# Kernel optimization log

Measured on AMD Instinct MI355X. Metric: run time of the kernel, lower is better.

Reference implementation:

```python
import jax, jax.numpy as jnp
import numpy as np

N, M, NBR = 20000, 12, 64
AF, ORIG, H, B, K = 256, 92, 256, 200, 50
N_CONV = 3
EPS = 1e-5


def _bn_train(x, gamma, beta):
    mu = x.mean(0)
    var = x.var(0)  # biased, matches torch BN normalization in train mode
    return (x - mu) * jax.lax.rsqrt(var + EPS) * gamma + beta


def _conv_layer(atom_in, nbr_fea, nbr_idx, w1, b1, w2, b2, gamma, beta):
    n, m = nbr_idx.shape
    m1 = m // 2
    atom_nbr = atom_in[nbr_idx]                     # [N, M, AF]
    atom_u = jnp.broadcast_to(atom_in[:, None, :], (n, m1, atom_in.shape[-1]))
    an1, an2 = atom_nbr[:, :m1], atom_nbr[:, m1:]
    nf1, nf2 = nbr_fea[:, :m1], nbr_fea[:, m1:]
    u1 = jnp.concatenate([atom_u, an1, nf1], axis=2)  # [N, M1, 2*AF+NBR]
    u2 = jnp.concatenate([atom_u, an2, nf2], axis=2)
    g1 = jax.nn.relu(jnp.einsum('nmf,fo->nmo', u1, w1) + b1)
    g2 = jax.nn.softplus(jnp.einsum('nmf,fo->nmo', u2, w1) + b1)
    nbr_sumed = g1.sum(1) + g2.sum(1)               # sum over all M neighbors, [N, 2*AF]
    nbr_sumed = nbr_sumed @ w2 + b2                 # [N, AF]
    nbr_sumed = _bn_train(nbr_sumed, gamma, beta)
    return jax.nn.softplus(atom_in + nbr_sumed)


def setup_inputs() -> dict:
    key = jax.random.key(0)
    ks = jax.random.split(key, 16)
    inp = {
        'atom_fea': jax.random.normal(ks[0], (N, ORIG), jnp.float32),
        'nbr_fea': jax.random.normal(ks[1], (N, M, NBR), jnp.float32),
        'nbr_fea_idx': jax.random.randint(ks[2], (N, M), 0, N),
        'M1_index': jax.random.randint(ks[3], (B * K,), 0, N),
        'seg_ids': jnp.repeat(jnp.arange(B), K),
        'm2_fea': jax.random.normal(ks[4], (B, 4), jnp.float32),
        'emb_w': jax.random.normal(ks[5], (ORIG, AF), jnp.float32) * 0.05,
        'emb_b': jnp.zeros((AF,), jnp.float32),
        'w1': jax.random.normal(ks[6], (N_CONV, 2 * AF + NBR, 2 * AF), jnp.float32) * 0.05,
        'b1': jnp.zeros((N_CONV, 2 * AF), jnp.float32),
        'w2': jax.random.normal(ks[7], (N_CONV, 2 * AF, AF), jnp.float32) * 0.05,
        'b2': jnp.zeros((N_CONV, AF), jnp.float32),
        'gamma': jnp.ones((N_CONV, AF), jnp.float32),
        'beta': jnp.zeros((N_CONV, AF), jnp.float32),
        'fc_w': jax.random.normal(ks[8], (AF + 4, H), jnp.float32) * 0.05,
        'fc_b': jnp.zeros((H,), jnp.float32),
        'out_w': jax.random.normal(ks[9], (H, 1), jnp.float32) * 0.05,
        'out_b': jnp.zeros((1,), jnp.float32),
    }
    return inp


def reference(atom_fea, nbr_fea, nbr_fea_idx, M1_index, seg_ids, m2_fea,
              emb_w, emb_b, w1, b1, w2, b2, gamma, beta,
              fc_w, fc_b, out_w, out_b):
    x = jax.nn.softplus(atom_fea @ emb_w + emb_b)           # [N, AF]
    for i in range(N_CONV):
        x = _conv_layer(x, nbr_fea, nbr_fea_idx, w1[i], b1[i], w2[i], b2[i], gamma[i], beta[i])
    m1_fea = x[M1_index]                                    # [B*K, AF]
    sums = jax.ops.segment_sum(m1_fea, seg_ids, num_segments=B)
    counts = jax.ops.segment_sum(jnp.ones((m1_fea.shape[0], 1), m1_fea.dtype), seg_ids, num_segments=B)
    crys = sums / counts                                    # per-crystal mean, [B, AF]
    crys = jnp.concatenate([crys, m2_fea], axis=1)          # [B, AF+4]
    h = jax.nn.softplus(jax.nn.softplus(crys) @ fc_w + fc_b)
    out = h @ out_w + out_b                                 # [B, 1]
    return out
```

## Files before the change

kernel.cpp:

```cpp
#include <hip/hip_runtime.h>
#include <hip/hip_bf16.h>


#define N_ATOM 20000
#define AF     256
#define F2     512
#define ORIG   92
#define ORIG_P 96
#define BB     200
#define KK     50
#define BN_EPS 1e-5f
#define ZS     132

#define OFF_B1   0
#define OFF_B2   1536
#define OFF_GAM  2304
#define OFF_BET  3072
#define OFF_EMBB 3840
#define OFF_FCB  4096
#define OFF_FCW  4352
#define OFF_OW   70912
#define OFF_OB   71168
#define OFF_M2   71169
#define N_SMALL  71969

#define S_AF   (N_ATOM * ORIG_P)
#define S_EMB  (AF * ORIG_P)
#define S_W12  (3 * 1024 * 256)
#define S_W1F  (3 * 512 * 64)
#define S_W2   (3 * AF * F2)
#define S_SM   N_SMALL
#define S_TOT  (S_AF + S_EMB + S_W12 + S_W1F + S_W2 + S_SM)

using bf16x8 = __attribute__((ext_vector_type(8))) short;
using f32x4  = __attribute__((ext_vector_type(4))) float;

__device__ __forceinline__ float bf2f(__hip_bfloat16 v) { return __bfloat162float(v); }
__device__ __forceinline__ __hip_bfloat16 f2bf(float v) { return __float2bfloat16(v); }
__device__ __forceinline__ unsigned short f2bfbits(float f) {
    unsigned u = __float_as_uint(f);
    u += 0x7fffu + ((u >> 16) & 1u);
    return (unsigned short)(u >> 16);
}
__device__ __forceinline__ float bfbits2f(unsigned short u) {
    return __uint_as_float(((unsigned)u) << 16);
}
__device__ __forceinline__ float softplus_f(float x) {
    return fmaxf(x, 0.f) + __logf(1.f + __expf(-fabsf(x)));
}
__device__ __forceinline__ float ld_any(const void* p, long idx, bool isf32) {
    return isf32 ? ((const float*)p)[idx] : bf2f(((const __hip_bfloat16*)p)[idx]);
}

__global__ void detect_dtype(const unsigned* __restrict__ gamma_raw,
                             unsigned* __restrict__ flag) {
    unsigned u = gamma_raw[0];
    flag[0] = ((u & 0xFFFFu) == 0u) ? 1u : 0u;
}

__global__ __launch_bounds__(256)
void prep_all(const void* af, const void* emb_w, const void* w1, const void* w2,
              const void* b1, const void* b2, const void* gam, const void* bet,
              const void* embb, const void* fcb, const void* fcw,
              const void* ow, const void* ob, const void* m2,
              const unsigned* __restrict__ dflag,
              __hip_bfloat16* __restrict__ af_pad, __hip_bfloat16* __restrict__ embT,
              __hip_bfloat16* __restrict__ w1T2, __hip_bfloat16* __restrict__ w1Tf,
              __hip_bfloat16* __restrict__ w2T, __hip_bfloat16* __restrict__ smalls) {
    bool isf32 = dflag[0] != 0u;
    int i = blockIdx.x * 256 + threadIdx.x;
    if (i < S_AF) {
        int r = i / ORIG_P, k = i - r * ORIG_P;
        af_pad[i] = (k < ORIG) ? f2bf(ld_any(af, (long)r * ORIG + k, isf32)) : f2bf(0.f);
        return;
    }
    i -= S_AF;
    if (i < S_EMB) {
        int n = i / ORIG_P, k = i - n * ORIG_P;
        embT[i] = (k < ORIG) ? f2bf(ld_any(emb_w, (long)k * AF + n, isf32)) : f2bf(0.f);
        return;
    }
    i -= S_EMB;
    if (i < S_W12) {
        int l = i / (1024 * 256); int rem = i - l * (1024 * 256);
        int c = rem / 256, k = rem - c * 256;
        long src = (c < 512) ? ((long)(l * 576 + k) * F2 + c)
                             : ((long)(l * 576 + 256 + k) * F2 + (c - 512));
        w1T2[i] = f2bf(ld_any(w1, src, isf32));
        return;
    }
    i -= S_W12;
    if (i < S_W1F) {
        int l = i / (512 * 64); int rem = i - l * (512 * 64);
        int c = rem / 64, k = rem - c * 64;
        w1Tf[i] = f2bf(ld_any(w1, (long)(l * 576 + 512 + k) * F2 + c, isf32));
        return;
    }
    i -= S_W1F;
    if (i < S_W2) {
        int l = i / (AF * F2); int rem = i - l * (AF * F2);
        int n = rem / F2, k = rem - n * F2;
        w2T[i] = f2bf(ld_any(w2, (long)(l * F2 + k) * AF + n, isf32));
        return;
    }
    i -= S_W2;
    if (i >= S_SM) return;
    float v;
    if      (i < OFF_B2)   v = ld_any(b1,   i - OFF_B1,  isf32);
    else if (i < OFF_GAM)  v = ld_any(b2,   i - OFF_B2,  isf32);
    else if (i < OFF_BET)  v = ld_any(gam,  i - OFF_GAM, isf32);
    else if (i < OFF_EMBB) v = ld_any(bet,  i - OFF_BET, isf32);
    else if (i < OFF_FCB)  v = ld_any(embb, i - OFF_EMBB,isf32);
    else if (i < OFF_OW)   v = (i < OFF_FCW) ? ld_any(fcb, i - OFF_FCB, isf32)
                                             : ld_any(fcw, i - OFF_FCW, isf32);
    else if (i < OFF_OB)   v = ld_any(ow,   i - OFF_OW,  isf32);
    else if (i < OFF_M2)   v = ld_any(ob,   i - OFF_OB,  isf32);
    else                   v = ld_any(m2,   i - OFF_M2,  isf32);
    smalls[i] = f2bf(v);
}

template <bool OUT_BF16>
__global__ __launch_bounds__(256)
void gemm_kernel(const __hip_bfloat16* __restrict__ A, int lda,
                 const __hip_bfloat16* __restrict__ BT, int ldb,
                 void* __restrict__ Cp, int M, int ldc, int K,
                 const __hip_bfloat16* __restrict__ bias, int act,
                 float* __restrict__ st) {
    __shared__ __align__(16) unsigned short sA[128 * 40];
    __shared__ __align__(16) unsigned short sB[128 * 40];
    __shared__ float sS[128], sS2[128];
    int tid  = threadIdx.x;
    int mt   = blockIdx.x, nt = blockIdx.y;
    int wave = tid >> 6, lane = tid & 63, q = lane >> 4, ln = lane & 15;
    int wr   = wave >> 1, wc = wave & 1;

    if (st && tid < 128) { sS[tid] = 0.f; sS2[tid] = 0.f; }

    f32x4 acc[4][4];
    for (int i = 0; i < 4; i++)
        for (int j = 0; j < 4; j++) acc[i][j] = (f32x4){0.f, 0.f, 0.f, 0.f};

    for (int k0 = 0; k0 < K; k0 += 32) {
        for (int i = tid; i < 512; i += 256) {
            int r = i >> 2, ch = i & 3;
            int row = mt * 128 + r;
            uint4 va = make_uint4(0u, 0u, 0u, 0u);
            if (row < M) va = *(const uint4*)(A + (size_t)row * lda + k0 + ch * 8);
            *(uint4*)(&sA[r * 40 + ch * 8]) = va;
            int n = nt * 128 + r;
            uint4 vb = *(const uint4*)(BT + (size_t)n * ldb + k0 + ch * 8);
            *(uint4*)(&sB[r * 40 + ch * 8]) = vb;
        }
        __syncthreads();
        bf16x8 af[4], bf[4];
        for (int i = 0; i < 4; i++)
            af[i] = *(const bf16x8*)(&sA[(wr * 64 + i * 16 + ln) * 40 + q * 8]);
        for (int j = 0; j < 4; j++)
            bf[j] = *(const bf16x8*)(&sB[(wc * 64 + j * 16 + ln) * 40 + q * 8]);
        for (int i = 0; i < 4; i++)
            for (int j = 0; j < 4; j++)
                acc[i][j] = __builtin_amdgcn_mfma_f32_16x16x32_bf16(af[i], bf[j], acc[i][j], 0, 0, 0);
        __syncthreads();
    }
    for (int j = 0; j < 4; j++) {
        int cl  = wc * 64 + j * 16 + ln;
        int col = nt * 128 + cl;
        float bv = bias ? bf2f(bias[col]) : 0.f;
        float ls = 0.f, ls2 = 0.f;
        for (int i = 0; i < 4; i++) {
            for (int r = 0; r < 4; r++) {
                int row = mt * 128 + wr * 64 + i * 16 + q * 4 + r;
                if (row >= M) continue;
                float v = acc[i][j][r] + bv;
                if (st) { ls += v; ls2 += v * v; }
                if (act == 1) v = softplus_f(v);
                if (OUT_BF16) ((__hip_bfloat16*)Cp)[(size_t)row * ldc + col] = f2bf(v);
                else          ((float*)Cp)[(size_t)row * ldc + col] = v;
            }
        }
        if (st) { atomicAdd(&sS[cl], ls); atomicAdd(&sS2[cl], ls2); }
    }
    if (st) {
        __syncthreads();
        if (tid < 128) {
            int col = nt * 128 + tid;
            atomicAdd(&st[col], sS[tid]);
            atomicAdd(&st[AF + col], sS2[tid]);
        }
    }
}

__global__ __launch_bounds__(256)
void conv_fused(const void* __restrict__ nf,
                const unsigned* __restrict__ dflag,
                const int* __restrict__ nidx,
                const __hip_bfloat16* __restrict__ xay,
                const __hip_bfloat16* __restrict__ b1l,
                const __hip_bfloat16* __restrict__ w1TfL,
                __hip_bfloat16* __restrict__ ns)
{
    __shared__ __align__(16) unsigned short sNF[48 * 72];
    __shared__ __align__(16) unsigned short sZ[48 * ZS];
    __shared__ int sIdx[48];

    int tid = threadIdx.x;
    int ab  = blockIdx.x * 4;

    if (dflag[0] == 0u) {
        const __hip_bfloat16* nfB = (const __hip_bfloat16*)nf;
        for (int i = tid; i < 48 * 8; i += 256) {
            int r = i >> 3, ch = i & 7;
            uint4 v = *(const uint4*)(nfB + (size_t)(ab * 12 + r) * 64 + ch * 8);
            *(uint4*)(&sNF[r * 72 + ch * 8]) = v;
        }
    } else {
        const float* nfF = (const float*)nf;
        for (int i = tid; i < 48 * 8; i += 256) {
            int r = i >> 3, ch = i & 7;
            const float* src = nfF + (size_t)(ab * 12 + r) * 64 + ch * 8;
            float4 v0 = *(const float4*)(src);
            float4 v1 = *(const float4*)(src + 4);
            unsigned short* d = &sNF[r * 72 + ch * 8];
            d[0] = f2bfbits(v0.x); d[1] = f2bfbits(v0.y);
            d[2] = f2bfbits(v0.z); d[3] = f2bfbits(v0.w);
            d[4] = f2bfbits(v1.x); d[5] = f2bfbits(v1.y);
            d[6] = f2bfbits(v1.z); d[7] = f2bfbits(v1.w);
        }
    }
    if (tid < 48) sIdx[tid] = nidx[ab * 12 + tid];
    __syncthreads();

    int wave = tid >> 6, lane = tid & 63, q = lane >> 4, ln = lane & 15;
    int c0 = wave * 32;
    int a  = tid >> 6, cg = lane;
    int n  = ab + a;

    for (int ct = 0; ct < 4; ct++) {
        int cb = ct * 128;
        bf16x8 bfr[2][2];
        for (int c2 = 0; c2 < 2; c2++)
            for (int ks = 0; ks < 2; ks++)
                bfr[c2][ks] = *(const bf16x8*)(w1TfL +
                    (size_t)(cb + c0 + c2 * 16 + ln) * 64 + ks * 32 + q * 8);

        f32x4 acc[3][2];
        for (int rt = 0; rt < 3; rt++)
            for (int c2 = 0; c2 < 2; c2++) acc[rt][c2] = (f32x4){0.f, 0.f, 0.f, 0.f};
        for (int rt = 0; rt < 3; rt++) {
            bf16x8 a0 = *(const bf16x8*)(&sNF[(rt * 16 + ln) * 72 + q * 8]);
            bf16x8 a1 = *(const bf16x8*)(&sNF[(rt * 16 + ln) * 72 + 32 + q * 8]);
            acc[rt][0] = __builtin_amdgcn_mfma_f32_16x16x32_bf16(a0, bfr[0][0], acc[rt][0], 0, 0, 0);
            acc[rt][0] = __builtin_amdgcn_mfma_f32_16x16x32_bf16(a1, bfr[0][1], acc[rt][0], 0, 0, 0);
            acc[rt][1] = __builtin_amdgcn_mfma_f32_16x16x32_bf16(a0, bfr[1][0], acc[rt][1], 0, 0, 0);
            acc[rt][1] = __builtin_amdgcn_mfma_f32_16x16x32_bf16(a1, bfr[1][1], acc[rt][1], 0, 0, 0);
        }
        __syncthreads();

        for (int rt = 0; rt < 3; rt++)
            for (int c2 = 0; c2 < 2; c2++)
                for (int r = 0; r < 4; r++)
                    sZ[(rt * 16 + q * 4 + r) * ZS + c0 + c2 * 16 + ln] = f2bfbits(acc[rt][c2][r]);
        __syncthreads();

        int gc = cb + cg * 2;
        unsigned xau = *(const unsigned*)(xay + (size_t)n * 1024 + gc);
        unsigned b1u = *(const unsigned*)(b1l + gc);
        float xa0 = bfbits2f((unsigned short)(xau & 0xffff)) +
                    bfbits2f((unsigned short)(b1u & 0xffff));
        float xa1 = bfbits2f((unsigned short)(xau >> 16)) +
                    bfbits2f((unsigned short)(b1u >> 16));
        float r0 = 0.f, r1 = 0.f;
#pragma unroll
        for (int m = 0; m < 12; m++) {
            int gi = sIdx[a * 12 + m];
            unsigned zz = *(const unsigned*)(&sZ[(a * 12 + m) * ZS + cg * 2]);
            unsigned yy = *(const unsigned*)(xay + (size_t)gi * 1024 + 512 + gc);
            float v0 = bfbits2f((unsigned short)(zz & 0xffff)) + xa0 +
                       bfbits2f((unsigned short)(yy & 0xffff));
            float v1 = bfbits2f((unsigned short)(zz >> 16)) + xa1 +
                       bfbits2f((unsigned short)(yy >> 16));
            if (m < 6) { v0 = fmaxf(v0, 0.f); v1 = fmaxf(v1, 0.f); }
            else       { v0 = softplus_f(v0); v1 = softplus_f(v1); }
            r0 += v0; r1 += v1;
        }
        unsigned o = (unsigned)f2bfbits(r0) | ((unsigned)f2bfbits(r1) << 16);
        *(unsigned*)(ns + (size_t)n * F2 + gc) = o;
    }
}

__global__ __launch_bounds__(256)
void bn_apply(const __hip_bfloat16* __restrict__ h2, const float* __restrict__ st,
              const __hip_bfloat16* __restrict__ x,
              const __hip_bfloat16* __restrict__ gamma,
              const __hip_bfloat16* __restrict__ beta,
              __hip_bfloat16* __restrict__ xo) {
    int i = (blockIdx.x * 256 + threadIdx.x) * 4;
    int c = i & 255;
    uint2 hv = *(const uint2*)(h2 + i);
    uint2 xv = *(const uint2*)(x + i);
    uint2 o;
    float r[4];
#pragma unroll
    for (int k = 0; k < 4; k++) {
        int cc = c + k;
        float mu  = st[cc] * (1.f / 20000.f);
        float var = fmaxf(st[AF + cc] * (1.f / 20000.f) - mu * mu, 0.f);
        unsigned hh = (k < 2) ? hv.x : hv.y;
        unsigned xx = (k < 2) ? xv.x : xv.y;
        float h  = bfbits2f((unsigned short)((k & 1) ? (hh >> 16) : (hh & 0xffff)));
        float xf = bfbits2f((unsigned short)((k & 1) ? (xx >> 16) : (xx & 0xffff)));
        float t = (h - mu) * rsqrtf(var + BN_EPS) * bf2f(gamma[cc]) + bf2f(beta[cc]);
        r[k] = softplus_f(xf + t);
    }
    o.x = (unsigned)f2bfbits(r[0]) | ((unsigned)f2bfbits(r[1]) << 16);
    o.y = (unsigned)f2bfbits(r[2]) | ((unsigned)f2bfbits(r[3]) << 16);
    *(uint2*)(xo + i) = o;
}

__global__ __launch_bounds__(256)
void readout(const __hip_bfloat16* __restrict__ x, const int* __restrict__ m1,
             const __hip_bfloat16* __restrict__ smalls,
             const unsigned* __restrict__ dflag,
             void* __restrict__ outp) {
    __shared__ float sc[AF + 4];
    __shared__ float sred[4];
    bool isf32 = dflag[0] != 0u;
    int b = blockIdx.x, tid = threadIdx.x;
    float s = 0.f;
    for (int j = 0; j < KK; j++) {
        int row = m1[b * KK + j];
        s += bf2f(x[(size_t)row * AF + tid]);
    }
    sc[tid] = softplus_f(s * (1.f / (float)KK));
    if (tid < 4) sc[AF + tid] = softplus_f(bf2f(smalls[OFF_M2 + b * 4 + tid]));
    __syncthreads();
    float acc = bf2f(smalls[OFF_FCB + tid]);
    for (int k = 0; k < AF + 4; k++) acc += sc[k] * bf2f(smalls[OFF_FCW + k * 256 + tid]);
    float h = softplus_f(acc);
    float v = h * bf2f(smalls[OFF_OW + tid]);
    for (int off = 32; off > 0; off >>= 1) v += __shfl_down(v, off);
    if ((tid & 63) == 0) sred[tid >> 6] = v;
    __syncthreads();
    if (tid == 0) {
        float o = sred[0] + sred[1] + sred[2] + sred[3] + bf2f(smalls[OFF_OB]);
        if (isf32) ((float*)outp)[b] = o;
        else       ((__hip_bfloat16*)outp)[b] = f2bf(o);
    }
}

extern "C" void kernel_launch(void* const* d_in, const int* in_sizes, int n_in,
                              void* d_out, int out_size, void* d_ws, size_t ws_size,
                              hipStream_t stream) {
    const void* atom_fea = d_in[0];
    const void* nbr_fea  = d_in[1];
    const int*  nbr_idx  = (const int*)d_in[2];
    const int*  m1_idx   = (const int*)d_in[3];
    const void* m2_fea = d_in[5];
    const void* emb_w  = d_in[6];
    const void* emb_b  = d_in[7];
    const void* w1     = d_in[8];
    const void* b1     = d_in[9];
    const void* w2     = d_in[10];
    const void* b2     = d_in[11];
    const void* gamma  = d_in[12];
    const void* beta   = d_in[13];
    const void* fc_w   = d_in[14];
    const void* fc_b   = d_in[15];
    const void* out_w  = d_in[16];
    const void* out_b  = d_in[17];

    char* ws = (char*)d_ws;
    size_t off = 0;
    auto alloc = [&](size_t bytes) -> char* {
        char* p = ws + off;
        off += (bytes + 255) & ~(size_t)255;
        return p;
    };
    __hip_bfloat16* w1T2   = (__hip_bfloat16*)alloc((size_t)S_W12 * 2);
    __hip_bfloat16* w1Tf   = (__hip_bfloat16*)alloc((size_t)S_W1F * 2);
    __hip_bfloat16* w2T    = (__hip_bfloat16*)alloc((size_t)S_W2 * 2);
    __hip_bfloat16* smalls = (__hip_bfloat16*)alloc((size_t)N_SMALL * 2);
    __hip_bfloat16* xb0    = (__hip_bfloat16*)alloc((size_t)N_ATOM * AF * 2);
    __hip_bfloat16* xb1    = (__hip_bfloat16*)alloc((size_t)N_ATOM * AF * 2);
    char*           regXY  = alloc((size_t)N_ATOM * 1024 * 2);
    char*           regZ   = alloc((size_t)N_ATOM * F2 * 2);
    float*          stats  = (float*)alloc((size_t)3 * 2 * AF * 4);
    unsigned*       dflag  = (unsigned*)alloc(256);

    __hip_bfloat16* xay    = (__hip_bfloat16*)regXY;
    __hip_bfloat16* h2     = (__hip_bfloat16*)regXY;
    __hip_bfloat16* af_pad = (__hip_bfloat16*)(regXY + (size_t)N_ATOM * F2 * 2);
    __hip_bfloat16* embT   = (__hip_bfloat16*)regZ;
    __hip_bfloat16* nsb    = (__hip_bfloat16*)regZ;

    detect_dtype<<<1, 1, 0, stream>>>((const unsigned*)gamma, dflag);
    (void)hipMemsetAsync(stats, 0, (size_t)3 * 2 * AF * 4, stream);

    prep_all<<<(S_TOT + 255) / 256, 256, 0, stream>>>(
        atom_fea, emb_w, w1, w2, b1, b2, gamma, beta, emb_b, fc_b, fc_w,
        out_w, out_b, m2_fea, dflag, af_pad, embT, w1T2, w1Tf, w2T, smalls);

    dim3 g_emb((N_ATOM + 127) / 128, 2);
    gemm_kernel<true><<<g_emb, 256, 0, stream>>>(af_pad, ORIG_P, embT, ORIG_P,
                                                 xb0, N_ATOM, AF, ORIG_P,
                                                 smalls + OFF_EMBB, 1, nullptr);

    __hip_bfloat16* xc = xb0;
    __hip_bfloat16* xn = xb1;
    for (int l = 0; l < 3; l++) {
        dim3 gxy((N_ATOM + 127) / 128, 8);
        gemm_kernel<true><<<gxy, 256, 0, stream>>>(xc, AF, w1T2 + (size_t)l * 1024 * 256, 256,
                                                   xay, N_ATOM, 1024, AF, nullptr, 0, nullptr);
        conv_fused<<<N_ATOM / 4, 256, 0, stream>>>(nbr_fea, dflag, nbr_idx, xay,
                                                   smalls + OFF_B1 + l * F2,
                                                   w1Tf + (size_t)l * 512 * 64, nsb);
        float* stl = stats + l * 2 * AF;
        dim3 gh2((N_ATOM + 127) / 128, 2);
        gemm_kernel<true><<<gh2, 256, 0, stream>>>(nsb, F2, w2T + (size_t)l * AF * F2, F2,
                                                   h2, N_ATOM, AF, F2,
                                                   smalls + OFF_B2 + l * AF, 0, stl);
        bn_apply<<<(N_ATOM * AF / 4) / 256, 256, 0, stream>>>(h2, stl, xc,
                                                              smalls + OFF_GAM + l * AF,
                                                              smalls + OFF_BET + l * AF, xn);
        __hip_bfloat16* t = xc; xc = xn; xn = t;
    }
    readout<<<BB, 256, 0, stream>>>(xc, m1_idx, smalls, dflag, d_out);
}
```

Measured before the change: 618.6 us.

## Pre-convert neighbor features once, widen conv gather and BN vector accesses

Adds a one-time kernel that converts nbr_fea to bf16 in workspace, so the three conv layers read half the bytes and skip per-layer conversion. Restructures conv_fused to compute two 128-column MFMA tiles into a wider shared buffer before each gather phase, which halves the barriers and lets each thread handle four columns with 8-byte gathers. bn_apply is widened to 16-byte loads and stores with 8 elements per thread. In exchange it needs extra workspace (with a fallback if there is not enough), uses more shared memory per block, and adds register pressure.

```diff
diff --git a/kernel.cpp b/kernel.cpp
--- a/kernel.cpp
+++ b/kernel.cpp
@@ -10,7 +10,7 @@
 #define BB     200
 #define KK     50
 #define BN_EPS 1e-5f
-#define ZS     132
+#define ZS2    268
 
 #define OFF_B1   0
 #define OFF_B2   1536
@@ -56,6 +56,21 @@
                              unsigned* __restrict__ flag) {
     unsigned u = gamma_raw[0];
     flag[0] = ((u & 0xFFFFu) == 0u) ? 1u : 0u;
+}
+
+__global__ __launch_bounds__(256) void prep_nf(const void* __restrict__ nf,
+                                               const unsigned* __restrict__ dflag,
+                                               unsigned* __restrict__ out) {
+    bool isf32 = dflag[0] != 0u;
+    int idx = blockIdx.x * 256 + threadIdx.x;
+    if (idx >= N_ATOM * 12 * 64 / 4) return;
+    if (isf32) {
+        float4 v = ((const float4*)nf)[idx];
+        out[idx * 2]     = (unsigned)f2bfbits(v.x) | ((unsigned)f2bfbits(v.y) << 16);
+        out[idx * 2 + 1] = (unsigned)f2bfbits(v.z) | ((unsigned)f2bfbits(v.w) << 16);
+    } else {
+        ((uint2*)out)[idx] = ((const uint2*)nf)[idx];
+    }
 }
 
 __global__ __launch_bounds__(256)
@@ -193,6 +208,7 @@
 __global__ __launch_bounds__(256)
 void conv_fused(const void* __restrict__ nf,
                 const unsigned* __restrict__ dflag,
+                int prepped,
                 const int* __restrict__ nidx,
                 const __hip_bfloat16* __restrict__ xay,
                 const __hip_bfloat16* __restrict__ b1l,
@@ -200,13 +216,13 @@
                 __hip_bfloat16* __restrict__ ns)
 {
     __shared__ __align__(16) unsigned short sNF[48 * 72];
-    __shared__ __align__(16) unsigned short sZ[48 * ZS];
+    __shared__ __align__(16) unsigned short sZ[48 * ZS2];
     __shared__ int sIdx[48];
 
     int tid = threadIdx.x;
     int ab  = blockIdx.x * 4;
 
-    if (dflag[0] == 0u) {
+    if (prepped || dflag[0] == 0u) {
         const __hip_bfloat16* nfB = (const __hip_bfloat16*)nf;
         for (int i = tid; i < 48 * 8; i += 256) {
             int r = i >> 3, ch = i & 7;
@@ -232,59 +248,76 @@
 
     int wave = tid >> 6, lane = tid & 63, q = lane >> 4, ln = lane & 15;
     int c0 = wave * 32;
-    int a  = tid >> 6, cg = lane;
-    int n  = ab + a;
-
-    for (int ct = 0; ct < 4; ct++) {
-        int cb = ct * 128;
-        bf16x8 bfr[2][2];
-        for (int c2 = 0; c2 < 2; c2++)
-            for (int ks = 0; ks < 2; ks++)
-                bfr[c2][ks] = *(const bf16x8*)(w1TfL +
-                    (size_t)(cb + c0 + c2 * 16 + ln) * 64 + ks * 32 + q * 8);
-
-        f32x4 acc[3][2];
-        for (int rt = 0; rt < 3; rt++)
-            for (int c2 = 0; c2 < 2; c2++) acc[rt][c2] = (f32x4){0.f, 0.f, 0.f, 0.f};
-        for (int rt = 0; rt < 3; rt++) {
-            bf16x8 a0 = *(const bf16x8*)(&sNF[(rt * 16 + ln) * 72 + q * 8]);
-            bf16x8 a1 = *(const bf16x8*)(&sNF[(rt * 16 + ln) * 72 + 32 + q * 8]);
-            acc[rt][0] = __builtin_amdgcn_mfma_f32_16x16x32_bf16(a0, bfr[0][0], acc[rt][0], 0, 0, 0);
-            acc[rt][0] = __builtin_amdgcn_mfma_f32_16x16x32_bf16(a1, bfr[0][1], acc[rt][0], 0, 0, 0);
-            acc[rt][1] = __builtin_amdgcn_mfma_f32_16x16x32_bf16(a0, bfr[1][0], acc[rt][1], 0, 0, 0);
-            acc[rt][1] = __builtin_amdgcn_mfma_f32_16x16x32_bf16(a1, bfr[1][1], acc[rt][1], 0, 0, 0);
+    int a = wave, half = lane >> 5, lc = lane & 31;
+    int n = ab + a;
+    int zc = half * 128 + lc * 4;
+
+    for (int tp = 0; tp < 2; tp++) {
+        if (tp) __syncthreads();
+        for (int t2 = 0; t2 < 2; t2++) {
+            int cb = (tp * 2 + t2) * 128;
+            bf16x8 bfr[2][2];
+            for (int c2 = 0; c2 < 2; c2++)
+                for (int ks = 0; ks < 2; ks++)
+                    bfr[c2][ks] = *(const bf16x8*)(w1TfL +
+                        (size_t)(cb + c0 + c2 * 16 + ln) * 64 + ks * 32 + q * 8);
+            f32x4 acc[3][2];
+            for (int rt = 0; rt < 3; rt++)
+                for (int c2 = 0; c2 < 2; c2++) acc[rt][c2] = (f32x4){0.f, 0.f, 0.f, 0.f};
+            for (int rt = 0; rt < 3; rt++) {
+                bf16x8 a0 = *(const bf16x8*)(&sNF[(rt * 16 + ln) * 72 + q * 8]);
+                bf16x8 a1 = *(const bf16x8*)(&sNF[(rt * 16 + ln) * 72 + 32 + q * 8]);
+                acc[rt][0] = __builtin_amdgcn_mfma_f32_16x16x32_bf16(a0, bfr[0][0], acc[rt][0], 0, 0, 0);
+                acc[rt][0] = __builtin_amdgcn_mfma_f32_16x16x32_bf16(a1, bfr[0][1], acc[rt][0], 0, 0, 0);
+                acc[rt][1] = __builtin_amdgcn_mfma_f32_16x16x32_bf16(a0, bfr[1][0], acc[rt][1], 0, 0, 0);
+                acc[rt][1] = __builtin_amdgcn_mfma_f32_16x16x32_bf16(a1, bfr[1][1], acc[rt][1], 0, 0, 0);
+            }
+            for (int rt = 0; rt < 3; rt++)
+                for (int c2 = 0; c2 < 2; c2++)
+                    for (int r = 0; r < 4; r++)
+                        sZ[(rt * 16 + q * 4 + r) * ZS2 + t2 * 128 + c0 + c2 * 16 + ln] =
+                            f2bfbits(acc[rt][c2][r]);
         }
         __syncthreads();
 
-        for (int rt = 0; rt < 3; rt++)
-            for (int c2 = 0; c2 < 2; c2++)
-                for (int r = 0; r < 4; r++)
-                    sZ[(rt * 16 + q * 4 + r) * ZS + c0 + c2 * 16 + ln] = f2bfbits(acc[rt][c2][r]);
-        __syncthreads();
-
-        int gc = cb + cg * 2;
-        unsigned xau = *(const unsigned*)(xay + (size_t)n * 1024 + gc);
-        unsigned b1u = *(const unsigned*)(b1l + gc);
-        float xa0 = bfbits2f((unsigned short)(xau & 0xffff)) +
-                    bfbits2f((unsigned short)(b1u & 0xffff));
-        float xa1 = bfbits2f((unsigned short)(xau >> 16)) +
-                    bfbits2f((unsigned short)(b1u >> 16));
-        float r0 = 0.f, r1 = 0.f;
+        int gc = tp * 256 + zc;
+        uint2 xau = *(const uint2*)(xay + (size_t)n * 1024 + gc);
+        uint2 b1u = *(const uint2*)(b1l + gc);
+        float xa0 = bfbits2f((unsigned short)(xau.x & 0xffff)) +
+                    bfbits2f((unsigned short)(b1u.x & 0xffff));
+        float xa1 = bfbits2f((unsigned short)(xau.x >> 16)) +
+                    bfbits2f((unsigned short)(b1u.x >> 16));
+        float xa2 = bfbits2f((unsigned short)(xau.y & 0xffff)) +
+                    bfbits2f((unsigned short)(b1u.y & 0xffff));
+        float xa3 = bfbits2f((unsigned short)(xau.y >> 16)) +
+                    bfbits2f((unsigned short)(b1u.y >> 16));
+        float r0 = 0.f, r1 = 0.f, r2 = 0.f, r3 = 0.f;
 #pragma unroll
         for (int m = 0; m < 12; m++) {
             int gi = sIdx[a * 12 + m];
-            unsigned zz = *(const unsigned*)(&sZ[(a * 12 + m) * ZS + cg * 2]);
-            unsigned yy = *(const unsigned*)(xay + (size_t)gi * 1024 + 512 + gc);
-            float v0 = bfbits2f((unsigned short)(zz & 0xffff)) + xa0 +
-                       bfbits2f((unsigned short)(yy & 0xffff));
-            float v1 = bfbits2f((unsigned short)(zz >> 16)) + xa1 +
-                       bfbits2f((unsigned short)(yy >> 16));
-            if (m < 6) { v0 = fmaxf(v0, 0.f); v1 = fmaxf(v1, 0.f); }
-            else       { v0 = softplus_f(v0); v1 = softplus_f(v1); }
-            r0 += v0; r1 += v1;
-        }
-        unsigned o = (unsigned)f2bfbits(r0) | ((unsigned)f2bfbits(r1) << 16);
-        *(unsigned*)(ns + (size_t)n * F2 + gc) = o;
+            uint2 zz = *(const uint2*)(&sZ[(a * 12 + m) * ZS2 + zc]);
+            uint2 yy = *(const uint2*)(xay + (size_t)gi * 1024 + 512 + gc);
+            float v0 = bfbits2f((unsigned short)(zz.x & 0xffff)) + xa0 +
+                       bfbits2f((unsigned short)(yy.x & 0xffff));
+            float v1 = bfbits2f((unsigned short)(zz.x >> 16)) + xa1 +
+                       bfbits2f((unsigned short)(yy.x >> 16));
+            float v2 = bfbits2f((unsigned short)(zz.y & 0xffff)) + xa2 +
+                       bfbits2f((unsigned short)(yy.y & 0xffff));
+            float v3 = bfbits2f((unsigned short)(zz.y >> 16)) + xa3 +
+                       bfbits2f((unsigned short)(yy.y >> 16));
+            if (m < 6) {
+                v0 = fmaxf(v0, 0.f); v1 = fmaxf(v1, 0.f);
+                v2 = fmaxf(v2, 0.f); v3 = fmaxf(v3, 0.f);
+            } else {
+                v0 = softplus_f(v0); v1 = softplus_f(v1);
+                v2 = softplus_f(v2); v3 = softplus_f(v3);
+            }
+            r0 += v0; r1 += v1; r2 += v2; r3 += v3;
+        }
+        uint2 o;
+        o.x = (unsigned)f2bfbits(r0) | ((unsigned)f2bfbits(r1) << 16);
+        o.y = (unsigned)f2bfbits(r2) | ((unsigned)f2bfbits(r3) << 16);
+        *(uint2*)(ns + (size_t)n * F2 + gc) = o;
     }
 }
 
@@ -294,27 +327,29 @@
               const __hip_bfloat16* __restrict__ gamma,
               const __hip_bfloat16* __restrict__ beta,
               __hip_bfloat16* __restrict__ xo) {
-    int i = (blockIdx.x * 256 + threadIdx.x) * 4;
+    int i = (blockIdx.x * 256 + threadIdx.x) * 8;
     int c = i & 255;
-    uint2 hv = *(const uint2*)(h2 + i);
-    uint2 xv = *(const uint2*)(x + i);
-    uint2 o;
-    float r[4];
+    uint4 hv = *(const uint4*)(h2 + i);
+    uint4 xv = *(const uint4*)(x + i);
+    unsigned hw[4] = {hv.x, hv.y, hv.z, hv.w};
+    unsigned xw[4] = {xv.x, xv.y, xv.z, xv.w};
+    unsigned ow[4];
+    float r[8];
 #pragma unroll
-    for (int k = 0; k < 4; k++) {
+    for (int k = 0; k < 8; k++) {
         int cc = c + k;
         float mu  = st[cc] * (1.f / 20000.f);
         float var = fmaxf(st[AF + cc] * (1.f / 20000.f) - mu * mu, 0.f);
-        unsigned hh = (k < 2) ? hv.x : hv.y;
-        unsigned xx = (k < 2) ? xv.x : xv.y;
+        unsigned hh = hw[k >> 1], xx = xw[k >> 1];
         float h  = bfbits2f((unsigned short)((k & 1) ? (hh >> 16) : (hh & 0xffff)));
         float xf = bfbits2f((unsigned short)((k & 1) ? (xx >> 16) : (xx & 0xffff)));
         float t = (h - mu) * rsqrtf(var + BN_EPS) * bf2f(gamma[cc]) + bf2f(beta[cc]);
         r[k] = softplus_f(xf + t);
     }
-    o.x = (unsigned)f2bfbits(r[0]) | ((unsigned)f2bfbits(r[1]) << 16);
-    o.y = (unsigned)f2bfbits(r[2]) | ((unsigned)f2bfbits(r[3]) << 16);
-    *(uint2*)(xo + i) = o;
+#pragma unroll
+    for (int k = 0; k < 4; k++)
+        ow[k] = (unsigned)f2bfbits(r[2 * k]) | ((unsigned)f2bfbits(r[2 * k + 1]) << 16);
+    *(uint4*)(xo + i) = make_uint4(ow[0], ow[1], ow[2], ow[3]);
 }
 
 __global__ __launch_bounds__(256)
@@ -386,6 +421,8 @@
     char*           regZ   = alloc((size_t)N_ATOM * F2 * 2);
     float*          stats  = (float*)alloc((size_t)3 * 2 * AF * 4);
     unsigned*       dflag  = (unsigned*)alloc(256);
+    char*           nfb    = alloc((size_t)N_ATOM * 12 * 64 * 2);
+    int use_nfb = (ws_size >= off) ? 1 : 0;
 
     __hip_bfloat16* xay    = (__hip_bfloat16*)regXY;
     __hip_bfloat16* h2     = (__hip_bfloat16*)regXY;
@@ -396,6 +433,9 @@
     detect_dtype<<<1, 1, 0, stream>>>((const unsigned*)gamma, dflag);
     (void)hipMemsetAsync(stats, 0, (size_t)3 * 2 * AF * 4, stream);
 
+    if (use_nfb)
+        prep_nf<<<(N_ATOM * 12 * 64 / 4 + 255) / 256, 256, 0, stream>>>(nbr_fea, dflag,
+                                                                        (unsigned*)nfb);
     prep_all<<<(S_TOT + 255) / 256, 256, 0, stream>>>(
         atom_fea, emb_w, w1, w2, b1, b2, gamma, beta, emb_b, fc_b, fc_w,
         out_w, out_b, m2_fea, dflag, af_pad, embT, w1T2, w1Tf, w2T, smalls);
@@ -404,6 +444,8 @@
     gemm_kernel<true><<<g_emb, 256, 0, stream>>>(af_pad, ORIG_P, embT, ORIG_P,
                                                  xb0, N_ATOM, AF, ORIG_P,
                                                  smalls + OFF_EMBB, 1, nullptr);
+
+    const void* nf_conv = use_nfb ? (const void*)nfb : nbr_fea;
 
     __hip_bfloat16* xc = xb0;
     __hip_bfloat16* xn = xb1;
@@ -411,7 +453,7 @@
         dim3 gxy((N_ATOM + 127) / 128, 8);
         gemm_kernel<true><<<gxy, 256, 0, stream>>>(xc, AF, w1T2 + (size_t)l * 1024 * 256, 256,
                                                    xay, N_ATOM, 1024, AF, nullptr, 0, nullptr);
-        conv_fused<<<N_ATOM / 4, 256, 0, stream>>>(nbr_fea, dflag, nbr_idx, xay,
+        conv_fused<<<N_ATOM / 4, 256, 0, stream>>>(nf_conv, dflag, use_nfb, nbr_idx, xay,
                                                    smalls + OFF_B1 + l * F2,
                                                    w1Tf + (size_t)l * 512 * 64, nsb);
         float* stl = stats + l * 2 * AF;
@@ -419,7 +461,7 @@
         gemm_kernel<true><<<gh2, 256, 0, stream>>>(nsb, F2, w2T + (size_t)l * AF * F2, F2,
                                                    h2, N_ATOM, AF, F2,
                                                    smalls + OFF_B2 + l * AF, 0, stl);
-        bn_apply<<<(N_ATOM * AF / 4) / 256, 256, 0, stream>>>(h2, stl, xc,
+        bn_apply<<<(N_ATOM * AF / 8) / 256, 256, 0, stream>>>(h2, stl, xc,
                                                               smalls + OFF_GAM + l * AF,
                                                               smalls + OFF_BET + l * AF, xn);
         __hip_bfloat16* t = xc; xc = xn; xn = t;
```

Measured after the change: 616.5 us. No clear change (-0.3%).
